# Kernel tuning notes

Measured on AMD Instinct MI355X. Metric: run time of the kernel, lower is better.

Reference implementation:

```python
import jax, jax.numpy as jnp
import numpy as np

N = 10000       # nodes
E = 320000      # edges (before self-loops)
IN = 16         # in_channels


def _p(key, shape, scale=0.1):
    return jax.random.normal(key, shape, jnp.float32) * scale


def setup_inputs() -> dict:
    key = jax.random.key(0)
    ks = jax.random.split(key, 26)
    d = {}
    d["x"] = jax.random.normal(ks[0], (N, IN), jnp.float32)
    d["edge_index"] = jax.random.randint(ks[1], (2, E), 0, N, jnp.int32)
    d["JetRawPt"] = jax.random.normal(ks[2], (N, 1), jnp.float32)
    # conv1: GATConv(16 -> 32, heads=8)
    d["W1"] = _p(ks[3], (IN, 8 * 32)); d["a1s"] = _p(ks[4], (8, 32)); d["a1d"] = _p(ks[5], (8, 32)); d["b1"] = jnp.zeros((256,), jnp.float32)
    # conv2: GATConv(256 -> 32, heads=8)
    d["W2"] = _p(ks[6], (256, 8 * 32)); d["a2s"] = _p(ks[7], (8, 32)); d["a2d"] = _p(ks[8], (8, 32)); d["b2"] = jnp.zeros((256,), jnp.float32)
    # conv3: GATConv(256 -> 64, heads=12)
    d["W3"] = _p(ks[9], (256, 12 * 64)); d["a3s"] = _p(ks[10], (12, 64)); d["a3d"] = _p(ks[11], (12, 64)); d["b3"] = jnp.zeros((768,), jnp.float32)
    # linear_final: 256+256+768=1280 -> 1
    d["Wf"] = _p(ks[12], (1280, 1)); d["bf"] = jnp.zeros((1,), jnp.float32)
    # MLP: (16+1)->128->64->1
    d["M1w"] = _p(ks[13], (IN + 1, 128)); d["M1b"] = jnp.zeros((128,), jnp.float32)
    d["M2w"] = _p(ks[14], (128, 64)); d["M2b"] = jnp.zeros((64,), jnp.float32)
    d["M3w"] = _p(ks[15], (64, 1)); d["M3b"] = jnp.zeros((1,), jnp.float32)
    return d


def gat_layer(x, src, dst, W, a_s, a_d, b, H, C):
    # PyG GATConv (eval mode, self-loops already appended to src/dst)
    h = (x @ W).reshape(-1, H, C)                      # [N, H, C]
    al = jnp.sum(h * a_s, axis=-1)                     # [N, H] src-side score
    ar = jnp.sum(h * a_d, axis=-1)                     # [N, H] dst-side score
    e = jax.nn.leaky_relu(al[src] + ar[dst], 0.2)      # [Etot, H]
    m = jax.ops.segment_max(e, dst, num_segments=N)    # segment softmax over incoming edges
    ex = jnp.exp(e - m[dst])
    s = jax.ops.segment_sum(ex, dst, num_segments=N)
    alpha = ex / s[dst]                                # [Etot, H]
    out = jax.ops.segment_sum(h[src] * alpha[:, :, None], dst, num_segments=N)  # [N, H, C]
    return out.reshape(-1, H * C) + b


def reference(x, edge_index, JetRawPt, W1, a1s, a1d, b1, W2, a2s, a2d, b2,
              W3, a3s, a3d, b3, Wf, bf, M1w, M1b, M2w, M2b, M3w, M3b):
    loops = jnp.arange(N, dtype=edge_index.dtype)
    src = jnp.concatenate([edge_index[0], loops])
    dst = jnp.concatenate([edge_index[1], loops])
    x1 = jax.nn.relu(gat_layer(x, src, dst, W1, a1s, a1d, b1, 8, 32))
    x2 = jax.nn.relu(gat_layer(x1, src, dst, W2, a2s, a2d, b2, 8, 32))
    x3 = jax.nn.relu(gat_layer(x2, src, dst, W3, a3s, a3d, b3, 12, 64))
    xc = jnp.concatenate([x1, x2, x3], axis=1)         # [N, 1280]
    out1 = jax.nn.sigmoid(xc @ Wf + bf)                # [N, 1]
    xm = jnp.concatenate([x, out1], axis=1)            # [N, 17]
    h = jax.nn.relu(xm @ M1w + M1b)
    h = jax.nn.relu(h @ M2w + M2b)
    out2 = jax.nn.sigmoid(h @ M3w + M3b)               # [N, 1]
    return (out1, out2)
```

## Files before the change

kernel.cpp:

```cpp
#include <hip/hip_runtime.h>
#include <math.h>


typedef unsigned short bf16_t;
typedef __attribute__((ext_vector_type(8))) short bf16x8;
typedef __attribute__((ext_vector_type(4))) float f32x4;
typedef __attribute__((ext_vector_type(2))) float f32x2;

__device__ inline float bf2f(bf16_t u) {
    union { unsigned int i; float f; } v; v.i = ((unsigned int)u) << 16; return v.f;
}
__device__ inline float u2f(unsigned int x) {
    union { unsigned int i; float f; } v; v.i = x; return v.f;
}
__device__ inline bf16_t f2bf(float f) {
    union { float f; unsigned int i; } v; v.f = f;
    unsigned int r = v.i + 0x7FFF + ((v.i >> 16) & 1);
    return (bf16_t)(r >> 16);
}


__global__ void count_edges(const int* __restrict__ ei, int E, int Nn,
                            int* __restrict__ counts) {
    int e = blockIdx.x * blockDim.x + threadIdx.x;
    if (e >= E + Nn) return;
    int dst = (e < E) ? ei[E + e] : (e - E);
    atomicAdd(&counts[dst], 1);
}

__global__ __launch_bounds__(1024) void scan_rowptr(const int* __restrict__ counts,
                                                    int* __restrict__ rowptr, int n) {
    const int IPT = (n + 1023) / 1024;
    int t = threadIdx.x;
    int base = t * IPT;
    int loc[16];
    int run = 0;
#pragma unroll
    for (int i = 0; i < 16; i++) {
        if (i >= IPT) break;
        int idx = base + i;
        int v = (idx < n) ? counts[idx] : 0;
        loc[i] = run;
        run += v;
    }
    int lane = t & 63, wid = t >> 6;
    int v = run;
    for (int off = 1; off < 64; off <<= 1) {
        int u = __shfl_up(v, off, 64);
        if (lane >= off) v += u;
    }
    __shared__ int wsum[16];
    __shared__ int woff[16];
    if (lane == 63) wsum[wid] = v;
    __syncthreads();
    if (t == 0) { int s = 0; for (int i = 0; i < 16; i++) { woff[i] = s; s += wsum[i]; } }
    __syncthreads();
    int excl = v - run + woff[wid];
#pragma unroll
    for (int i = 0; i < 16; i++) {
        if (i >= IPT) break;
        int idx = base + i;
        if (idx < n) rowptr[idx] = excl + loc[i];
    }
    if (t == 1023) rowptr[n] = excl + run;
}

__global__ void fill_edges(const int* __restrict__ ei, int E, int Nn,
                           const int* __restrict__ rowptr, int* __restrict__ cursor,
                           int* __restrict__ edge_src) {
    int e = blockIdx.x * blockDim.x + threadIdx.x;
    if (e >= E + Nn) return;
    int src, dst;
    if (e < E) { src = ei[e]; dst = ei[E + e]; }
    else       { src = e - E; dst = src; }
    int pos = atomicAdd(&cursor[dst], 1);
    edge_src[rowptr[dst] + pos] = src;
}

__global__ __launch_bounds__(256) void transpose_cast2(const float* __restrict__ W2,
                                                       bf16_t* __restrict__ Wt2,
                                                       const float* __restrict__ W3,
                                                       bf16_t* __restrict__ Wt3) {
    __shared__ float tile[16][17];
    const float* W; bf16_t* Wt; int Nc, n0;
    if (blockIdx.y < 16) { W = W2; Wt = Wt2; Nc = 256; n0 = blockIdx.y * 16; }
    else                 { W = W3; Wt = Wt3; Nc = 768; n0 = (blockIdx.y - 16) * 16; }
    int k0 = blockIdx.x * 16;
    int tx = threadIdx.x & 15, ty = threadIdx.x >> 4;
    tile[ty][tx] = W[(size_t)(k0 + ty) * Nc + n0 + tx];
    __syncthreads();
    Wt[(size_t)(n0 + ty) * 256 + k0 + tx] = f2bf(tile[tx][ty]);
}

__global__ __launch_bounds__(256) void gemm_f32_sc(const float* __restrict__ A,
                                                   const float* __restrict__ B,
                                                   bf16_t* __restrict__ Cm,
                                                   const float* __restrict__ a_s,
                                                   const float* __restrict__ a_d,
                                                   float* __restrict__ al,
                                                   float* __restrict__ ar,
                                                   int M, int K, int Nc, int H) {
    __shared__ float As[16][64];
    __shared__ float Bs[16][64];
    int t  = threadIdx.x;
    int tx = t & 15, ty = t >> 4;
    int row0 = blockIdx.y * 64, col0 = blockIdx.x * 64;
    int a_r = t >> 2, a_c = (t & 3) * 4;
    int b_r = t >> 4, b_c = (t & 15) * 4;

    float acc[4][4];
#pragma unroll
    for (int i = 0; i < 4; i++)
#pragma unroll
        for (int j = 0; j < 4; j++) acc[i][j] = 0.f;

    for (int kt = 0; kt < K; kt += 16) {
        float4 av = make_float4(0.f, 0.f, 0.f, 0.f);
        int gr = row0 + a_r;
        if (gr < M) av = *(const float4*)(A + (size_t)gr * K + kt + a_c);
        As[a_c + 0][a_r] = av.x;
        As[a_c + 1][a_r] = av.y;
        As[a_c + 2][a_r] = av.z;
        As[a_c + 3][a_r] = av.w;
        float4 bv = *(const float4*)(B + (size_t)(kt + b_r) * Nc + col0 + b_c);
        *(float4*)&Bs[b_r][b_c] = bv;
        __syncthreads();
#pragma unroll
        for (int k = 0; k < 16; k++) {
            float4 a4 = *(const float4*)&As[k][ty * 4];
            float4 b4 = *(const float4*)&Bs[k][tx * 4];
            float aa[4] = {a4.x, a4.y, a4.z, a4.w};
            float bb[4] = {b4.x, b4.y, b4.z, b4.w};
#pragma unroll
            for (int i = 0; i < 4; i++)
#pragma unroll
                for (int j = 0; j < 4; j++) acc[i][j] += aa[i] * bb[j];
        }
        __syncthreads();
    }
    float4 asv = *(const float4*)(a_s + col0 + tx * 4);
    float4 adv = *(const float4*)(a_d + col0 + tx * 4);
#pragma unroll
    for (int i = 0; i < 4; i++) {
        int gr = row0 + ty * 4 + i;
        float sa = acc[i][0] * asv.x + acc[i][1] * asv.y + acc[i][2] * asv.z + acc[i][3] * asv.w;
        float sd = acc[i][0] * adv.x + acc[i][1] * adv.y + acc[i][2] * adv.z + acc[i][3] * adv.w;
#pragma unroll
        for (int off = 4; off > 0; off >>= 1) {
            sa += __shfl_xor(sa, off, 64);
            sd += __shfl_xor(sd, off, 64);
        }
        if ((tx == 0 || tx == 8) && gr < M) {
            int h = (col0 >> 5) + (tx >> 3);
            al[gr * H + h] = sa;
            ar[gr * H + h] = sd;
        }
        if (gr < M) {
            ushort4 v;
            v.x = f2bf(acc[i][0]); v.y = f2bf(acc[i][1]);
            v.z = f2bf(acc[i][2]); v.w = f2bf(acc[i][3]);
            *(ushort4*)(Cm + (size_t)gr * Nc + col0 + tx * 4) = v;
        }
    }
}

template <int C_>
__global__ __launch_bounds__(256) void gemm_mfma_sc(const bf16_t* __restrict__ A,
                                                    const bf16_t* __restrict__ Bt,
                                                    bf16_t* __restrict__ Cm,
                                                    const float* __restrict__ a_s,
                                                    const float* __restrict__ a_d,
                                                    float* __restrict__ al,
                                                    float* __restrict__ ar,
                                                    int M, int K, int Nc, int H) {
    int wave = threadIdx.x >> 6, lane = threadIdx.x & 63;
    int quad = lane >> 4, l16 = lane & 15;
    int m0 = blockIdx.y * 128 + wave * 32;
    int n0 = blockIdx.x * 64;

    f32x4 acc[2][4];
    f32x4 z = {0.f, 0.f, 0.f, 0.f};
#pragma unroll
    for (int i = 0; i < 2; i++)
#pragma unroll
        for (int j = 0; j < 4; j++) acc[i][j] = z;

    int r0 = m0 + l16;       if (r0 >= M) r0 = M - 1;
    int r1 = m0 + 16 + l16;  if (r1 >= M) r1 = M - 1;
    const bf16_t* Ap0 = A + (size_t)r0 * K + quad * 8;
    const bf16_t* Ap1 = A + (size_t)r1 * K + quad * 8;
    const bf16_t* Bp0 = Bt + (size_t)(n0 + 0  + l16) * K + quad * 8;
    const bf16_t* Bp1 = Bt + (size_t)(n0 + 16 + l16) * K + quad * 8;
    const bf16_t* Bp2 = Bt + (size_t)(n0 + 32 + l16) * K + quad * 8;
    const bf16_t* Bp3 = Bt + (size_t)(n0 + 48 + l16) * K + quad * 8;

    for (int kt = 0; kt < K; kt += 32) {
        bf16x8 a0 = *(const bf16x8*)(Ap0 + kt);
        bf16x8 a1 = *(const bf16x8*)(Ap1 + kt);
        bf16x8 b0 = *(const bf16x8*)(Bp0 + kt);
        bf16x8 b1 = *(const bf16x8*)(Bp1 + kt);
        bf16x8 b2 = *(const bf16x8*)(Bp2 + kt);
        bf16x8 b3 = *(const bf16x8*)(Bp3 + kt);
        acc[0][0] = __builtin_amdgcn_mfma_f32_16x16x32_bf16(a0, b0, acc[0][0], 0, 0, 0);
        acc[1][0] = __builtin_amdgcn_mfma_f32_16x16x32_bf16(a1, b0, acc[1][0], 0, 0, 0);
        acc[0][1] = __builtin_amdgcn_mfma_f32_16x16x32_bf16(a0, b1, acc[0][1], 0, 0, 0);
        acc[1][1] = __builtin_amdgcn_mfma_f32_16x16x32_bf16(a1, b1, acc[1][1], 0, 0, 0);
        acc[0][2] = __builtin_amdgcn_mfma_f32_16x16x32_bf16(a0, b2, acc[0][2], 0, 0, 0);
        acc[1][2] = __builtin_amdgcn_mfma_f32_16x16x32_bf16(a1, b2, acc[1][2], 0, 0, 0);
        acc[0][3] = __builtin_amdgcn_mfma_f32_16x16x32_bf16(a0, b3, acc[0][3], 0, 0, 0);
        acc[1][3] = __builtin_amdgcn_mfma_f32_16x16x32_bf16(a1, b3, acc[1][3], 0, 0, 0);
    }

    float asv[4], adv[4];
#pragma unroll
    for (int j = 0; j < 4; j++) {
        asv[j] = a_s[n0 + j * 16 + l16];
        adv[j] = a_d[n0 + j * 16 + l16];
    }
#pragma unroll
    for (int i = 0; i < 2; i++)
#pragma unroll
        for (int r = 0; r < 4; r++) {
            int gr = m0 + i * 16 + quad * 4 + r;
            if (C_ == 64) {
                float sa = acc[i][0][r] * asv[0] + acc[i][1][r] * asv[1]
                         + acc[i][2][r] * asv[2] + acc[i][3][r] * asv[3];
                float sd = acc[i][0][r] * adv[0] + acc[i][1][r] * adv[1]
                         + acc[i][2][r] * adv[2] + acc[i][3][r] * adv[3];
#pragma unroll
                for (int off = 8; off > 0; off >>= 1) {
                    sa += __shfl_xor(sa, off, 64);
                    sd += __shfl_xor(sd, off, 64);
                }
                if (l16 == 0 && gr < M) {
                    int h = n0 >> 6;
                    al[gr * H + h] = sa;
                    ar[gr * H + h] = sd;
                }
            } else {
                float saA = acc[i][0][r] * asv[0] + acc[i][1][r] * asv[1];
                float saB = acc[i][2][r] * asv[2] + acc[i][3][r] * asv[3];
                float sdA = acc[i][0][r] * adv[0] + acc[i][1][r] * adv[1];
                float sdB = acc[i][2][r] * adv[2] + acc[i][3][r] * adv[3];
#pragma unroll
                for (int off = 8; off > 0; off >>= 1) {
                    saA += __shfl_xor(saA, off, 64);
                    saB += __shfl_xor(saB, off, 64);
                    sdA += __shfl_xor(sdA, off, 64);
                    sdB += __shfl_xor(sdB, off, 64);
                }
                if (l16 == 0 && gr < M) {
                    int h = n0 >> 5;
                    al[gr * H + h]     = saA;
                    ar[gr * H + h]     = sdA;
                    al[gr * H + h + 1] = saB;
                    ar[gr * H + h + 1] = sdB;
                }
            }
        }
#pragma unroll
    for (int i = 0; i < 2; i++)
#pragma unroll
        for (int j = 0; j < 4; j++)
#pragma unroll
            for (int r = 0; r < 4; r++) {
                int gr = m0 + i * 16 + quad * 4 + r;
                if (gr < M) Cm[(size_t)gr * Nc + n0 + j * 16 + l16] = f2bf(acc[i][j][r]);
            }
}

template <int H>
__global__ __launch_bounds__(256) void alpha_node(const float* __restrict__ al,
                                                  const float* __restrict__ ar,
                                                  const int* __restrict__ rowptr,
                                                  const int* __restrict__ esrc,
                                                  float* __restrict__ alpha,
                                                  int n, int Etot) {
    int pair = (blockIdx.x * blockDim.x + threadIdx.x) >> 6;
    int lane = threadIdx.x & 63;
    int node = pair * 2 + (lane >> 5);
    if (node >= n) return;
    int lane32 = lane & 31;

    float arv[H];
#pragma unroll
    for (int h4 = 0; h4 < H; h4 += 4) {
        float4 t = *(const float4*)(ar + (size_t)node * H + h4);
        arv[h4] = t.x; arv[h4 + 1] = t.y; arv[h4 + 2] = t.z; arv[h4 + 3] = t.w;
    }
    int beg = rowptr[node], end = rowptr[node + 1];
    float p0[H], p1[H], s[H];
#pragma unroll
    for (int h = 0; h < H; h++) { p0[h] = 0.f; p1[h] = 0.f; s[h] = 0.f; }

    int j0 = beg + lane32;
    if (j0 < end) {
        const float* alr = al + (size_t)esrc[j0] * H;
#pragma unroll
        for (int h4 = 0; h4 < H; h4 += 4) {
            float4 t = *(const float4*)(alr + h4);
            float e;
            e = t.x + arv[h4];     e = fmaxf(e, 0.2f * e); p0[h4]     = __expf(fminf(e, 60.f));
            e = t.y + arv[h4 + 1]; e = fmaxf(e, 0.2f * e); p0[h4 + 1] = __expf(fminf(e, 60.f));
            e = t.z + arv[h4 + 2]; e = fmaxf(e, 0.2f * e); p0[h4 + 2] = __expf(fminf(e, 60.f));
            e = t.w + arv[h4 + 3]; e = fmaxf(e, 0.2f * e); p0[h4 + 3] = __expf(fminf(e, 60.f));
        }
#pragma unroll
        for (int h = 0; h < H; h++) s[h] += p0[h];
    }
    int j1 = j0 + 32;
    if (j1 < end) {
        const float* alr = al + (size_t)esrc[j1] * H;
#pragma unroll
        for (int h4 = 0; h4 < H; h4 += 4) {
            float4 t = *(const float4*)(alr + h4);
            float e;
            e = t.x + arv[h4];     e = fmaxf(e, 0.2f * e); p1[h4]     = __expf(fminf(e, 60.f));
            e = t.y + arv[h4 + 1]; e = fmaxf(e, 0.2f * e); p1[h4 + 1] = __expf(fminf(e, 60.f));
            e = t.z + arv[h4 + 2]; e = fmaxf(e, 0.2f * e); p1[h4 + 2] = __expf(fminf(e, 60.f));
            e = t.w + arv[h4 + 3]; e = fmaxf(e, 0.2f * e); p1[h4 + 3] = __expf(fminf(e, 60.f));
        }
#pragma unroll
        for (int h = 0; h < H; h++) s[h] += p1[h];
    }
    for (int j = j0 + 64; j < end; j += 32) {
        const float* alr = al + (size_t)esrc[j] * H;
#pragma unroll
        for (int h = 0; h < H; h++) {
            float e = alr[h] + arv[h];
            e = fmaxf(e, 0.2f * e);
            float p = __expf(fminf(e, 60.f));
            alpha[(size_t)h * Etot + j] = p;
            s[h] += p;
        }
    }
#pragma unroll
    for (int h = 0; h < H; h++) {
        float v = s[h];
#pragma unroll
        for (int off = 16; off > 0; off >>= 1) v += __shfl_xor(v, off, 64);
        s[h] = 1.f / v;
    }
    if (j0 < end) {
#pragma unroll
        for (int h = 0; h < H; h++) alpha[(size_t)h * Etot + j0] = p0[h] * s[h];
    }
    if (j1 < end) {
#pragma unroll
        for (int h = 0; h < H; h++) alpha[(size_t)h * Etot + j1] = p1[h] * s[h];
    }
    for (int j = j0 + 64; j < end; j += 32) {
#pragma unroll
        for (int h = 0; h < H; h++) alpha[(size_t)h * Etot + j] *= s[h];
    }
}

template <int HC_, int C>
__global__ __launch_bounds__(256) void gat_agg(
    const bf16_t* __restrict__ hbuf, const float* __restrict__ alpha,
    const int* __restrict__ rowptr, const int* __restrict__ esrc,
    const float* __restrict__ bias, bf16_t* __restrict__ outb,
    int n, int Etot, int nodeblocks) {
    int group = blockIdx.x / nodeblocks;
    int nb    = blockIdx.x - group * nodeblocks;
    int node  = nb * 4 + (threadIdx.x >> 6);
    if (node >= n) return;
    int lane = threadIdx.x & 63;
    int sub  = lane >> 4;
    int cl   = lane & 15;
    int gc   = group * 128 + cl * 8;
    int head = gc / C;
    const bf16_t* hb = hbuf + gc;
    const float*  ap = alpha + (size_t)head * Etot;

    f32x2 acc2[4];
    f32x2 z2 = {0.f, 0.f};
#pragma unroll
    for (int i = 0; i < 4; i++) acc2[i] = z2;

    int beg = rowptr[node], end = rowptr[node + 1];
    int deg = end - beg;

    int e0 = 0, e1 = 0;
    {
        int i0 = beg + lane;
        if (i0 < end) e0 = esrc[i0];
        int i1 = beg + 64 + lane;
        if (i1 < end) e1 = esrc[i1];
    }
    int npre  = deg < 128 ? deg : 128;
    int nfull = npre >> 3;

    if (nfull > 0) {
        int s0 = __shfl(e0, sub, 64);
        int s1 = __shfl(e0, sub + 4, 64);
        float a0 = ap[beg + sub], a1 = ap[beg + sub + 4];
        bf16x8 u0 = *(const bf16x8*)(hb + (size_t)s0 * HC_);
        bf16x8 u1 = *(const bf16x8*)(hb + (size_t)s1 * HC_);
        for (int it = 1; it < nfull; ++it) {
            int kb = it * 8;
            int esel = (kb < 64) ? e0 : e1;
            int t0 = __shfl(esel, (kb + sub) & 63, 64);
            int t1 = __shfl(esel, (kb + sub + 4) & 63, 64);
            float b0v = ap[beg + kb + sub], b1v = ap[beg + kb + sub + 4];
            bf16x8 v0 = *(const bf16x8*)(hb + (size_t)t0 * HC_);
            bf16x8 v1 = *(const bf16x8*)(hb + (size_t)t1 * HC_);
            const unsigned int* d0 = (const unsigned int*)&u0;
            const unsigned int* d1 = (const unsigned int*)&u1;
            f32x2 a0v = {a0, a0}, a1v = {a1, a1};
#pragma unroll
            for (int i = 0; i < 4; i++) {
                f32x2 w0 = {u2f(d0[i] << 16), u2f(d0[i] & 0xffff0000u)};
                f32x2 w1 = {u2f(d1[i] << 16), u2f(d1[i] & 0xffff0000u)};
                acc2[i] += a0v * w0;
                acc2[i] += a1v * w1;
            }
            u0 = v0; u1 = v1; a0 = b0v; a1 = b1v;
        }
        const unsigned int* d0 = (const unsigned int*)&u0;
        const unsigned int* d1 = (const unsigned int*)&u1;
        f32x2 a0v = {a0, a0}, a1v = {a1, a1};
#pragma unroll
        for (int i = 0; i < 4; i++) {
            f32x2 w0 = {u2f(d0[i] << 16), u2f(d0[i] & 0xffff0000u)};
            f32x2 w1 = {u2f(d1[i] << 16), u2f(d1[i] & 0xffff0000u)};
            acc2[i] += a0v * w0;
            acc2[i] += a1v * w1;
        }
    }
    for (int j = beg + (nfull << 3) + sub; j < end; j += 4) {
        int s0 = esrc[j];
        float a0 = ap[j];
        bf16x8 u0 = *(const bf16x8*)(hb + (size_t)s0 * HC_);
        const unsigned int* d0 = (const unsigned int*)&u0;
        f32x2 a0v = {a0, a0};
#pragma unroll
        for (int i = 0; i < 4; i++) {
            f32x2 w0 = {u2f(d0[i] << 16), u2f(d0[i] & 0xffff0000u)};
            acc2[i] += a0v * w0;
        }
    }
    float acc[8] = {acc2[0].x, acc2[0].y, acc2[1].x, acc2[1].y,
                    acc2[2].x, acc2[2].y, acc2[3].x, acc2[3].y};
#pragma unroll
    for (int i = 0; i < 8; i++) {
        acc[i] += __shfl_xor(acc[i], 16, 64);
        acc[i] += __shfl_xor(acc[i], 32, 64);
    }
    if (sub == 0) {
        float4 b0 = *(const float4*)(bias + gc);
        float4 b1 = *(const float4*)(bias + gc + 4);
        float bb[8] = {b0.x, b0.y, b0.z, b0.w, b1.x, b1.y, b1.z, b1.w};
        bf16x8 outv;
        unsigned short* ov = (unsigned short*)&outv;
#pragma unroll
        for (int i = 0; i < 8; i++) ov[i] = f2bf(fmaxf(acc[i] + bb[i], 0.f));
        *(bf16x8*)(outb + (size_t)node * HC_ + gc) = outv;
    }
}

__global__ __launch_bounds__(256) void head_fused(
    const float* __restrict__ x, const bf16_t* __restrict__ x1b,
    const bf16_t* __restrict__ x2b, const bf16_t* __restrict__ x3b,
    const float* __restrict__ Wf, const float* __restrict__ bfc,
    const float* __restrict__ M1w, const float* __restrict__ M1b,
    const float* __restrict__ M2w, const float* __restrict__ M2b,
    const float* __restrict__ M3w, const float* __restrict__ M3b,
    float* __restrict__ out1, float* __restrict__ out2, int n) {
    __shared__ float h1s[4][128];
    int w    = threadIdx.x >> 6;
    int lane = threadIdx.x & 63;
    int node = blockIdx.x * 4 + w;
    bool valid = node < n;
    int nd = valid ? node : 0;

    float s = 0.f;
    {
        ushort4 u = *(const ushort4*)(x1b + (size_t)nd * 256 + lane * 4);
        const float* wv = Wf + lane * 4;
        s += bf2f(u.x) * wv[0] + bf2f(u.y) * wv[1] + bf2f(u.z) * wv[2] + bf2f(u.w) * wv[3];
    }
    {
        ushort4 u = *(const ushort4*)(x2b + (size_t)nd * 256 + lane * 4);
        const float* wv = Wf + 256 + lane * 4;
        s += bf2f(u.x) * wv[0] + bf2f(u.y) * wv[1] + bf2f(u.z) * wv[2] + bf2f(u.w) * wv[3];
    }
#pragma unroll
    for (int i = 0; i < 3; i++) {
        int k = i * 256 + lane * 4;
        ushort4 u = *(const ushort4*)(x3b + (size_t)nd * 768 + k);
        const float* wv = Wf + 512 + k;
        s += bf2f(u.x) * wv[0] + bf2f(u.y) * wv[1] + bf2f(u.z) * wv[2] + bf2f(u.w) * wv[3];
    }
#pragma unroll
    for (int off = 32; off > 0; off >>= 1) s += __shfl_xor(s, off, 64);
    float so = 1.f / (1.f + __expf(-(s + bfc[0])));
    if (lane == 0 && valid) out1[node] = so;

    float xm[17];
#pragma unroll
    for (int k = 0; k < 16; k++) xm[k] = x[nd * 16 + k];
    xm[16] = so;

    float a0 = M1b[lane], a1 = M1b[lane + 64];
#pragma unroll
    for (int k = 0; k < 17; k++) {
        a0 += xm[k] * M1w[k * 128 + lane];
        a1 += xm[k] * M1w[k * 128 + lane + 64];
    }
    h1s[w][lane]      = fmaxf(a0, 0.f);
    h1s[w][lane + 64] = fmaxf(a1, 0.f);
    __syncthreads();

    float b0 = M2b[lane];
#pragma unroll 16
    for (int k = 0; k < 128; k++) b0 += h1s[w][k] * M2w[k * 64 + lane];
    b0 = fmaxf(b0, 0.f);

    float p = b0 * M3w[lane];
#pragma unroll
    for (int off = 32; off > 0; off >>= 1) p += __shfl_xor(p, off, 64);
    if (lane == 0 && valid) out2[node] = 1.f / (1.f + __expf(-(p + M3b[0])));
}

extern "C" void kernel_launch(void* const* d_in, const int* in_sizes, int n_in,
                              void* d_out, int out_size, void* d_ws, size_t ws_size,
                              hipStream_t stream) {
    const float* x   = (const float*)d_in[0];
    const int*   ei  = (const int*)d_in[1];
    const float* W1  = (const float*)d_in[3];
    const float* a1s = (const float*)d_in[4];
    const float* a1d = (const float*)d_in[5];
    const float* b1  = (const float*)d_in[6];
    const float* W2  = (const float*)d_in[7];
    const float* a2s = (const float*)d_in[8];
    const float* a2d = (const float*)d_in[9];
    const float* b2  = (const float*)d_in[10];
    const float* W3  = (const float*)d_in[11];
    const float* a3s = (const float*)d_in[12];
    const float* a3d = (const float*)d_in[13];
    const float* b3  = (const float*)d_in[14];
    const float* Wf  = (const float*)d_in[15];
    const float* bf  = (const float*)d_in[16];
    const float* M1w = (const float*)d_in[17];
    const float* M1b = (const float*)d_in[18];
    const float* M2w = (const float*)d_in[19];
    const float* M2b = (const float*)d_in[20];
    const float* M3w = (const float*)d_in[21];
    const float* M3b = (const float*)d_in[22];

    const int N = in_sizes[0] / 16;
    const int E = in_sizes[1] / 2;
    const int Etot = E + N;

    char* base = (char*)d_ws;
    size_t off = 0;
    auto carve = [&](size_t bytes) {
        char* p = base + off;
        off = (off + bytes + 255) & ~(size_t)255;
        return p;
    };
    bf16_t* hbuf   = (bf16_t*)carve((size_t)N * 768 * 2);
    bf16_t* x1b    = (bf16_t*)carve((size_t)N * 256 * 2);
    bf16_t* x2b    = (bf16_t*)carve((size_t)N * 256 * 2);
    bf16_t* x3b    = (bf16_t*)carve((size_t)N * 768 * 2);
    bf16_t* Wt2    = (bf16_t*)carve((size_t)256 * 256 * 2);
    bf16_t* Wt3    = (bf16_t*)carve((size_t)256 * 768 * 2);
    float*  al     = (float*)carve((size_t)N * 12 * 4);
    float*  ar     = (float*)carve((size_t)N * 12 * 4);
    float*  alphab = (float*)carve((size_t)Etot * 12 * 4);
    int*    rowptr = (int*)carve((size_t)(N + 1) * 4);
    int*    cnt2   = (int*)carve((size_t)(2 * N) * 4);
    int*    counts = cnt2;
    int*    cursor = cnt2 + N;
    int*    esrc   = (int*)carve((size_t)Etot * 4);
    (void)ws_size;

    float* out1 = (float*)d_out;
    float* out2 = (float*)d_out + N;

    const int TB = 256;
    int eb = (Etot + TB - 1) / TB;
    int nodeblocks = (N + 3) / 4;
    int alphablocks = (N + 7) / 8;

    hipMemsetAsync(cnt2, 0, (size_t)(2 * N) * 4, stream);
    count_edges<<<eb, TB, 0, stream>>>(ei, E, N, counts);
    scan_rowptr<<<1, 1024, 0, stream>>>(counts, rowptr, N);
    fill_edges<<<eb, TB, 0, stream>>>(ei, E, N, rowptr, cursor, esrc);
    transpose_cast2<<<dim3(16, 64), TB, 0, stream>>>(W2, Wt2, W3, Wt3);

    gemm_f32_sc<<<dim3(4, (N + 63) / 64), TB, 0, stream>>>(x, W1, hbuf, a1s, a1d, al, ar, N, 16, 256, 8);
    alpha_node<8><<<alphablocks, TB, 0, stream>>>(al, ar, rowptr, esrc, alphab, N, Etot);
    gat_agg<256, 32><<<2 * nodeblocks, TB, 0, stream>>>(hbuf, alphab, rowptr, esrc, b1, x1b, N, Etot, nodeblocks);

    gemm_mfma_sc<32><<<dim3(4, (N + 127) / 128), TB, 0, stream>>>(x1b, Wt2, hbuf, a2s, a2d, al, ar, N, 256, 256, 8);
    alpha_node<8><<<alphablocks, TB, 0, stream>>>(al, ar, rowptr, esrc, alphab, N, Etot);
    gat_agg<256, 32><<<2 * nodeblocks, TB, 0, stream>>>(hbuf, alphab, rowptr, esrc, b2, x2b, N, Etot, nodeblocks);

    gemm_mfma_sc<64><<<dim3(12, (N + 127) / 128), TB, 0, stream>>>(x2b, Wt3, hbuf, a3s, a3d, al, ar, N, 256, 768, 12);
    alpha_node<12><<<alphablocks, TB, 0, stream>>>(al, ar, rowptr, esrc, alphab, N, Etot);
    gat_agg<768, 64><<<6 * nodeblocks, TB, 0, stream>>>(hbuf, alphab, rowptr, esrc, b3, x3b, N, Etot, nodeblocks);

    head_fused<<<nodeblocks, TB, 0, stream>>>(x, x1b, x2b, x3b, Wf, bf,
                                              M1w, M1b, M2w, M2b, M3w, M3b, out1, out2, N);
}
```

Measured before the change: 327.4 us.

## Fuse attention softmax into GAT aggregation, computing unnormalized weights in LDS

Removes the separate alpha_node kernel and its Etot x H alpha buffer. Each aggregation wave now computes the exp scores for its own head group, stores up to 128 of them in shared memory, reduces the softmax denominator across the wave, and applies normalization once at the output. The goal is to eliminate three launches and the global write and read of alpha. In exchange, score computation is repeated across column groups (6 groups for layer 3), and edges past 128 are recomputed inline.

```diff
diff --git a/kernel.cpp b/kernel.cpp
--- a/kernel.cpp
+++ b/kernel.cpp
@@ -269,114 +269,21 @@
             }
 }
 
-template <int H>
-__global__ __launch_bounds__(256) void alpha_node(const float* __restrict__ al,
-                                                  const float* __restrict__ ar,
-                                                  const int* __restrict__ rowptr,
-                                                  const int* __restrict__ esrc,
-                                                  float* __restrict__ alpha,
-                                                  int n, int Etot) {
-    int pair = (blockIdx.x * blockDim.x + threadIdx.x) >> 6;
-    int lane = threadIdx.x & 63;
-    int node = pair * 2 + (lane >> 5);
-    if (node >= n) return;
-    int lane32 = lane & 31;
-
-    float arv[H];
-#pragma unroll
-    for (int h4 = 0; h4 < H; h4 += 4) {
-        float4 t = *(const float4*)(ar + (size_t)node * H + h4);
-        arv[h4] = t.x; arv[h4 + 1] = t.y; arv[h4 + 2] = t.z; arv[h4 + 3] = t.w;
-    }
-    int beg = rowptr[node], end = rowptr[node + 1];
-    float p0[H], p1[H], s[H];
-#pragma unroll
-    for (int h = 0; h < H; h++) { p0[h] = 0.f; p1[h] = 0.f; s[h] = 0.f; }
-
-    int j0 = beg + lane32;
-    if (j0 < end) {
-        const float* alr = al + (size_t)esrc[j0] * H;
-#pragma unroll
-        for (int h4 = 0; h4 < H; h4 += 4) {
-            float4 t = *(const float4*)(alr + h4);
-            float e;
-            e = t.x + arv[h4];     e = fmaxf(e, 0.2f * e); p0[h4]     = __expf(fminf(e, 60.f));
-            e = t.y + arv[h4 + 1]; e = fmaxf(e, 0.2f * e); p0[h4 + 1] = __expf(fminf(e, 60.f));
-            e = t.z + arv[h4 + 2]; e = fmaxf(e, 0.2f * e); p0[h4 + 2] = __expf(fminf(e, 60.f));
-            e = t.w + arv[h4 + 3]; e = fmaxf(e, 0.2f * e); p0[h4 + 3] = __expf(fminf(e, 60.f));
-        }
-#pragma unroll
-        for (int h = 0; h < H; h++) s[h] += p0[h];
-    }
-    int j1 = j0 + 32;
-    if (j1 < end) {
-        const float* alr = al + (size_t)esrc[j1] * H;
-#pragma unroll
-        for (int h4 = 0; h4 < H; h4 += 4) {
-            float4 t = *(const float4*)(alr + h4);
-            float e;
-            e = t.x + arv[h4];     e = fmaxf(e, 0.2f * e); p1[h4]     = __expf(fminf(e, 60.f));
-            e = t.y + arv[h4 + 1]; e = fmaxf(e, 0.2f * e); p1[h4 + 1] = __expf(fminf(e, 60.f));
-            e = t.z + arv[h4 + 2]; e = fmaxf(e, 0.2f * e); p1[h4 + 2] = __expf(fminf(e, 60.f));
-            e = t.w + arv[h4 + 3]; e = fmaxf(e, 0.2f * e); p1[h4 + 3] = __expf(fminf(e, 60.f));
-        }
-#pragma unroll
-        for (int h = 0; h < H; h++) s[h] += p1[h];
-    }
-    for (int j = j0 + 64; j < end; j += 32) {
-        const float* alr = al + (size_t)esrc[j] * H;
-#pragma unroll
-        for (int h = 0; h < H; h++) {
-            float e = alr[h] + arv[h];
-            e = fmaxf(e, 0.2f * e);
-            float p = __expf(fminf(e, 60.f));
-            alpha[(size_t)h * Etot + j] = p;
-            s[h] += p;
-        }
-    }
-#pragma unroll
-    for (int h = 0; h < H; h++) {
-        float v = s[h];
-#pragma unroll
-        for (int off = 16; off > 0; off >>= 1) v += __shfl_xor(v, off, 64);
-        s[h] = 1.f / v;
-    }
-    if (j0 < end) {
-#pragma unroll
-        for (int h = 0; h < H; h++) alpha[(size_t)h * Etot + j0] = p0[h] * s[h];
-    }
-    if (j1 < end) {
-#pragma unroll
-        for (int h = 0; h < H; h++) alpha[(size_t)h * Etot + j1] = p1[h] * s[h];
-    }
-    for (int j = j0 + 64; j < end; j += 32) {
-#pragma unroll
-        for (int h = 0; h < H; h++) alpha[(size_t)h * Etot + j] *= s[h];
-    }
-}
-
-template <int HC_, int C>
-__global__ __launch_bounds__(256) void gat_agg(
-    const bf16_t* __restrict__ hbuf, const float* __restrict__ alpha,
-    const int* __restrict__ rowptr, const int* __restrict__ esrc,
-    const float* __restrict__ bias, bf16_t* __restrict__ outb,
-    int n, int Etot, int nodeblocks) {
+template <int HC_, int C, int H>
+__global__ __launch_bounds__(256) void gat_agg_fused(
+    const bf16_t* __restrict__ hbuf, const float* __restrict__ al,
+    const float* __restrict__ ar, const int* __restrict__ rowptr,
+    const int* __restrict__ esrc, const float* __restrict__ bias,
+    bf16_t* __restrict__ outb, int n, int nodeblocks) {
+    constexpr int HPG = 128 / C;
+    __shared__ float plds[4][128 * HPG];
     int group = blockIdx.x / nodeblocks;
     int nb    = blockIdx.x - group * nodeblocks;
-    int node  = nb * 4 + (threadIdx.x >> 6);
+    int wv    = threadIdx.x >> 6;
+    int node  = nb * 4 + wv;
     if (node >= n) return;
-    int lane = threadIdx.x & 63;
-    int sub  = lane >> 4;
-    int cl   = lane & 15;
-    int gc   = group * 128 + cl * 8;
-    int head = gc / C;
-    const bf16_t* hb = hbuf + gc;
-    const float*  ap = alpha + (size_t)head * Etot;
-
-    f32x2 acc2[4];
-    f32x2 z2 = {0.f, 0.f};
-#pragma unroll
-    for (int i = 0; i < 4; i++) acc2[i] = z2;
+    int lane  = threadIdx.x & 63;
+    int ghead = group * HPG;
 
     int beg = rowptr[node], end = rowptr[node + 1];
     int deg = end - beg;
@@ -388,13 +295,71 @@
         int i1 = beg + 64 + lane;
         if (i1 < end) e1 = esrc[i1];
     }
+
+    float arv[HPG];
+#pragma unroll
+    for (int t = 0; t < HPG; t++) arv[t] = ar[(size_t)node * H + ghead + t];
+    float s[HPG];
+#pragma unroll
+    for (int t = 0; t < HPG; t++) s[t] = 0.f;
+    float* pw = plds[wv];
+    for (int k = 0; k < deg; k += 64) {
+        int j = k + lane;
+        if (j < deg) {
+            int src = (k == 0) ? e0 : ((k == 64) ? e1 : esrc[beg + j]);
+            const float* alr = al + (size_t)src * H + ghead;
+            float p[HPG];
+#pragma unroll
+            for (int t = 0; t < HPG; t++) {
+                float e = alr[t] + arv[t];
+                e = fmaxf(e, 0.2f * e);
+                p[t] = __expf(fminf(e, 60.f));
+                s[t] += p[t];
+            }
+            if (j < 128) {
+#pragma unroll
+                for (int t = 0; t < HPG; t++) pw[j * HPG + t] = p[t];
+            }
+        }
+    }
+#pragma unroll
+    for (int t = 0; t < HPG; t++) {
+        float v = s[t];
+#pragma unroll
+        for (int off = 32; off > 0; off >>= 1) v += __shfl_xor(v, off, 64);
+        s[t] = 1.f / v;
+    }
+
+    int sub = lane >> 4, cl = lane & 15;
+    int gc  = group * 128 + cl * 8;
+    int t_local = (cl * 8) / C;
+    float inv_local, arv_local;
+    if (HPG == 2) {
+        inv_local = t_local ? s[1] : s[0];
+        arv_local = t_local ? arv[1] : arv[0];
+    } else {
+        float iv0 = t_local & 1 ? s[1] : s[0];
+        float iv1 = t_local & 1 ? s[3] : s[2];
+        inv_local = (t_local & 2) ? iv1 : iv0;
+        float av0 = t_local & 1 ? arv[1] : arv[0];
+        float av1 = t_local & 1 ? arv[3] : arv[2];
+        arv_local = (t_local & 2) ? av1 : av0;
+    }
+    const bf16_t* hb = hbuf + gc;
+
+    f32x2 acc2[4];
+    f32x2 z2 = {0.f, 0.f};
+#pragma unroll
+    for (int i = 0; i < 4; i++) acc2[i] = z2;
+
     int npre  = deg < 128 ? deg : 128;
     int nfull = npre >> 3;
 
     if (nfull > 0) {
         int s0 = __shfl(e0, sub, 64);
         int s1 = __shfl(e0, sub + 4, 64);
-        float a0 = ap[beg + sub], a1 = ap[beg + sub + 4];
+        float a0 = pw[sub * HPG + t_local];
+        float a1 = pw[(sub + 4) * HPG + t_local];
         bf16x8 u0 = *(const bf16x8*)(hb + (size_t)s0 * HC_);
         bf16x8 u1 = *(const bf16x8*)(hb + (size_t)s1 * HC_);
         for (int it = 1; it < nfull; ++it) {
@@ -402,7 +367,8 @@
             int esel = (kb < 64) ? e0 : e1;
             int t0 = __shfl(esel, (kb + sub) & 63, 64);
             int t1 = __shfl(esel, (kb + sub + 4) & 63, 64);
-            float b0v = ap[beg + kb + sub], b1v = ap[beg + kb + sub + 4];
+            float b0v = pw[(kb + sub) * HPG + t_local];
+            float b1v = pw[(kb + sub + 4) * HPG + t_local];
             bf16x8 v0 = *(const bf16x8*)(hb + (size_t)t0 * HC_);
             bf16x8 v1 = *(const bf16x8*)(hb + (size_t)t1 * HC_);
             const unsigned int* d0 = (const unsigned int*)&u0;
@@ -430,7 +396,15 @@
     }
     for (int j = beg + (nfull << 3) + sub; j < end; j += 4) {
         int s0 = esrc[j];
-        float a0 = ap[j];
+        int jl = j - beg;
+        float a0;
+        if (jl < 128) {
+            a0 = pw[jl * HPG + t_local];
+        } else {
+            float e = al[(size_t)s0 * H + ghead + t_local] + arv_local;
+            e = fmaxf(e, 0.2f * e);
+            a0 = __expf(fminf(e, 60.f));
+        }
         bf16x8 u0 = *(const bf16x8*)(hb + (size_t)s0 * HC_);
         const unsigned int* d0 = (const unsigned int*)&u0;
         f32x2 a0v = {a0, a0};
@@ -454,7 +428,7 @@
         bf16x8 outv;
         unsigned short* ov = (unsigned short*)&outv;
 #pragma unroll
-        for (int i = 0; i < 8; i++) ov[i] = f2bf(fmaxf(acc[i] + bb[i], 0.f));
+        for (int i = 0; i < 8; i++) ov[i] = f2bf(fmaxf(acc[i] * inv_local + bb[i], 0.f));
         *(bf16x8*)(outb + (size_t)node * HC_ + gc) = outv;
     }
 }
@@ -568,7 +542,6 @@
     bf16_t* Wt3    = (bf16_t*)carve((size_t)256 * 768 * 2);
     float*  al     = (float*)carve((size_t)N * 12 * 4);
     float*  ar     = (float*)carve((size_t)N * 12 * 4);
-    float*  alphab = (float*)carve((size_t)Etot * 12 * 4);
     int*    rowptr = (int*)carve((size_t)(N + 1) * 4);
     int*    cnt2   = (int*)carve((size_t)(2 * N) * 4);
     int*    counts = cnt2;
@@ -582,7 +555,6 @@
     const int TB = 256;
     int eb = (Etot + TB - 1) / TB;
     int nodeblocks = (N + 3) / 4;
-    int alphablocks = (N + 7) / 8;
 
     hipMemsetAsync(cnt2, 0, (size_t)(2 * N) * 4, stream);
     count_edges<<<eb, TB, 0, stream>>>(ei, E, N, counts);
@@ -591,16 +563,13 @@
     transpose_cast2<<<dim3(16, 64), TB, 0, stream>>>(W2, Wt2, W3, Wt3);
 
     gemm_f32_sc<<<dim3(4, (N + 63) / 64), TB, 0, stream>>>(x, W1, hbuf, a1s, a1d, al, ar, N, 16, 256, 8);
-    alpha_node<8><<<alphablocks, TB, 0, stream>>>(al, ar, rowptr, esrc, alphab, N, Etot);
-    gat_agg<256, 32><<<2 * nodeblocks, TB, 0, stream>>>(hbuf, alphab, rowptr, esrc, b1, x1b, N, Etot, nodeblocks);
+    gat_agg_fused<256, 32, 8><<<2 * nodeblocks, TB, 0, stream>>>(hbuf, al, ar, rowptr, esrc, b1, x1b, N, nodeblocks);
 
     gemm_mfma_sc<32><<<dim3(4, (N + 127) / 128), TB, 0, stream>>>(x1b, Wt2, hbuf, a2s, a2d, al, ar, N, 256, 256, 8);
-    alpha_node<8><<<alphablocks, TB, 0, stream>>>(al, ar, rowptr, esrc, alphab, N, Etot);
-    gat_agg<256, 32><<<2 * nodeblocks, TB, 0, stream>>>(hbuf, alphab, rowptr, esrc, b2, x2b, N, Etot, nodeblocks);
+    gat_agg_fused<256, 32, 8><<<2 * nodeblocks, TB, 0, stream>>>(hbuf, al, ar, rowptr, esrc, b2, x2b, N, nodeblocks);
 
     gemm_mfma_sc<64><<<dim3(12, (N + 127) / 128), TB, 0, stream>>>(x2b, Wt3, hbuf, a3s, a3d, al, ar, N, 256, 768, 12);
-    alpha_node<12><<<alphablocks, TB, 0, stream>>>(al, ar, rowptr, esrc, alphab, N, Etot);
-    gat_agg<768, 64><<<6 * nodeblocks, TB, 0, stream>>>(hbuf, alphab, rowptr, esrc, b3, x3b, N, Etot, nodeblocks);
+    gat_agg_fused<768, 64, 12><<<6 * nodeblocks, TB, 0, stream>>>(hbuf, al, ar, rowptr, esrc, b3, x3b, N, nodeblocks);
 
     head_fused<<<nodeblocks, TB, 0, stream>>>(x, x1b, x2b, x3b, Wf, bf,
                                               M1w, M1b, M2w, M2b, M3w, M3b, out1, out2, N);
```

Result: faster. 312.7 us (-4.5%).
